# Performance work log

Measured on AMD Instinct MI355X. Metric: run time of the kernel, lower is better.

Reference implementation:

```python
import jax, jax.numpy as jnp
import numpy as np

B, S, D, H = 4, 2048, 1024, 16
HS = D // H  # head_size = 64
EPS = 1e-5


def setup_inputs() -> dict:
    key = jax.random.key(0)
    ks = jax.random.split(key, 10)
    s = 0.02
    return {
        "v": jax.random.normal(ks[0], (B, S, D), dtype=jnp.float32),
        "k": jax.random.normal(ks[1], (B, S, D), dtype=jnp.float32),
        "q": jax.random.normal(ks[2], (B, S, D), dtype=jnp.float32),
        "mask": jnp.triu(jnp.ones((S, S), dtype=bool), k=1),  # True = masked (causal)
        "ln_g": jnp.ones((D,), dtype=jnp.float32),
        "ln_b": jnp.zeros((D,), dtype=jnp.float32),
        # per-head projections, stacked: [H, D, HS]
        "Wq": jax.random.normal(ks[3], (H, D, HS), dtype=jnp.float32) * s,
        "Wk": jax.random.normal(ks[4], (H, D, HS), dtype=jnp.float32) * s,
        "Wv": jax.random.normal(ks[5], (H, D, HS), dtype=jnp.float32) * s,
        "Wp": jax.random.normal(ks[6], (D, D), dtype=jnp.float32) * s,
        "bp": jnp.zeros((D,), dtype=jnp.float32),
    }


def _layernorm(x, g, b):
    mu = jnp.mean(x, axis=-1, keepdims=True)
    var = jnp.var(x, axis=-1, keepdims=True)
    return (x - mu) * jax.lax.rsqrt(var + EPS) * g + b


def reference(v, k, q, mask, ln_g, ln_b, Wq, Wk, Wv, Wp, bp):
    v = _layernorm(v, ln_g, ln_b)
    k = _layernorm(k, ln_g, ln_b)
    q = _layernorm(q, ln_g, ln_b)
    # per-head projections: [B,S,D] x [H,D,E] -> [B,H,S,E]
    qh = jnp.einsum("bsd,hde->bhse", q, Wq)
    kh = jnp.einsum("bsd,hde->bhse", k, Wk)
    vh = jnp.einsum("bsd,hde->bhse", v, Wv)
    # NOTE: original scales by full embedding_dim C**-0.5 (not head_size)
    scale = jnp.float32(D) ** -0.5
    w = jnp.einsum("bhqe,bhke->bhqk", qh, kh) * scale
    w = jnp.where(mask, -jnp.inf, w)
    w = jax.nn.softmax(w, axis=-1)
    out = jnp.einsum("bhqk,bhke->bhqe", w, vh)  # [B,H,S,E]
    out = out.transpose(0, 2, 1, 3).reshape(B, S, D)  # concat heads
    return out @ Wp.T + bp
```

## Files before the change

### kernel.cpp

```cpp
#include <hip/hip_runtime.h>
#include <hip/hip_bf16.h>
#include <cstdint>
#include <cstddef>

#define Bq 4
#define Sq 2048
#define Dq 1024
#define Hq 16
#define HSq 64
#define Kc 1024

typedef short short8 __attribute__((ext_vector_type(8)));
typedef float f32x4 __attribute__((ext_vector_type(4)));

__device__ __forceinline__ unsigned short f2bf(float f){
  __hip_bfloat16 h = __float2bfloat16(f);
  return __builtin_bit_cast(unsigned short, h);
}

__device__ __forceinline__ float exp2hw(float x){
  float r;
  asm("v_exp_f32 %0, %1" : "=v"(r) : "v"(x));
  return r;
}
__device__ __forceinline__ unsigned cvtpk(float lo, float hi){
  unsigned r;
  asm("v_cvt_pk_bf16_f32 %0, %1, %2" : "=v"(r) : "v"(lo), "v"(hi));
  return r;
}
__device__ __forceinline__ float rcphw(float x){
  float r;
  asm("v_rcp_f32 %0, %1" : "=v"(r) : "v"(x));
  return r;
}

__device__ __forceinline__ void gl_lds16(const void* g, void* l){
  __builtin_amdgcn_global_load_lds((const __attribute__((address_space(1))) void*)(g),
                                   (__attribute__((address_space(3))) void*)(l), 16, 0, 0);
}

__global__ __launch_bounds__(256) void ln3_kernel(const float* __restrict__ v,
                                                  const float* __restrict__ k,
                                                  const float* __restrict__ q,
                                                  const float* __restrict__ g,
                                                  const float* __restrict__ bta,
                                                  short* __restrict__ vo,
                                                  short* __restrict__ ko,
                                                  short* __restrict__ qo){
  const int which = blockIdx.y;
  const float* x = (which==0) ? v : (which==1) ? k : q;
  short* out     = (which==0) ? vo : (which==1) ? ko : qo;
  const int row = blockIdx.x;
  const float* xr = x + (size_t)row * Dq;
  const int t = threadIdx.x;
  float4 vv = reinterpret_cast<const float4*>(xr)[t];
  float s  = vv.x + vv.y + vv.z + vv.w;
  float ss = vv.x*vv.x + vv.y*vv.y + vv.z*vv.z + vv.w*vv.w;
  #pragma unroll
  for (int o = 32; o >= 1; o >>= 1){ s += __shfl_xor(s, o); ss += __shfl_xor(ss, o); }
  __shared__ float red[8];
  const int wid = t >> 6;
  if ((t & 63) == 0){ red[wid] = s; red[4+wid] = ss; }
  __syncthreads();
  s  = red[0]+red[1]+red[2]+red[3];
  ss = red[4]+red[5]+red[6]+red[7];
  const float mu   = s * (1.0f/Dq);
  const float var  = ss * (1.0f/Dq) - mu*mu;
  const float rstd = rsqrtf(var + 1e-5f);
  float4 gv = reinterpret_cast<const float4*>(g)[t];
  float4 bv = reinterpret_cast<const float4*>(bta)[t];
  ushort4 o4;
  o4.x = f2bf((vv.x-mu)*rstd*gv.x + bv.x);
  o4.y = f2bf((vv.y-mu)*rstd*gv.y + bv.y);
  o4.z = f2bf((vv.z-mu)*rstd*gv.z + bv.z);
  o4.w = f2bf((vv.w-mu)*rstd*gv.w + bv.w);
  reinterpret_cast<ushort4*>(out + (size_t)row*Dq)[t] = o4;
}

__global__ __launch_bounds__(256) void cvt_kernel(const float* __restrict__ in,
                                                  short* __restrict__ out, int n4){
  int i = blockIdx.x*256 + threadIdx.x;
  if (i < n4){
    float4 v = reinterpret_cast<const float4*>(in)[i];
    ushort4 o; o.x=f2bf(v.x); o.y=f2bf(v.y); o.z=f2bf(v.z); o.w=f2bf(v.w);
    reinterpret_cast<ushort4*>(out)[i] = o;
  }
}

__global__ __launch_bounds__(256) void trcvt3_kernel(const float* __restrict__ Wq,
                                                     const float* __restrict__ Wk,
                                                     const float* __restrict__ Wv,
                                                     short* __restrict__ wqt,
                                                     short* __restrict__ wkt,
                                                     short* __restrict__ wvt){
  const int z = blockIdx.z;
  const float* Wsrc = (z==0) ? Wq : (z==1) ? Wk : Wv;
  short* Wdst       = (z==0) ? wqt : (z==1) ? wkt : wvt;
  const float scl   = (z==0) ? (0.03125f * 1.44269504f) : 1.0f;
  const int h = blockIdx.y, kt = blockIdx.x, tid = threadIdx.x;
  __shared__ short t[64][68];
  const float* src = Wsrc + ((size_t)h*Kc + (size_t)kt*64) * HSq;
  #pragma unroll
  for (int c=0;c<4;c++){
    int lin = c*256 + tid;
    int kr = lin >> 4;
    int e4 = (lin & 15) * 4;
    float4 vv = *reinterpret_cast<const float4*>(&src[(size_t)kr*HSq + e4]);
    t[e4+0][kr] = (short)f2bf(vv.x*scl);
    t[e4+1][kr] = (short)f2bf(vv.y*scl);
    t[e4+2][kr] = (short)f2bf(vv.z*scl);
    t[e4+3][kr] = (short)f2bf(vv.w*scl);
  }
  __syncthreads();
  short* dst = Wdst + (size_t)h*HSq*Kc + (size_t)kt*64;
  #pragma unroll
  for (int c=0;c<4;c++){
    int lin = c*256 + tid;
    int er = lin >> 4;
    int k4 = (lin & 15) * 4;
    ushort4 o;
    o.x = (unsigned short)t[er][k4+0];
    o.y = (unsigned short)t[er][k4+1];
    o.z = (unsigned short)t[er][k4+2];
    o.w = (unsigned short)t[er][k4+3];
    *reinterpret_cast<ushort4*>(&dst[(size_t)er*Kc + k4]) = o;
  }
}

__global__ __launch_bounds__(256) void proj3_kernel(
    const short* __restrict__ qn, const short* __restrict__ kn, const short* __restrict__ vn,
    const short* __restrict__ wqt, const short* __restrict__ wkt, const short* __restrict__ wvt,
    short* __restrict__ qh, short* __restrict__ kh, short* __restrict__ vhT)
{
  const int z = blockIdx.y;
  const short* A  = (z==0) ? qn  : (z==1) ? kn  : vn;
  const short* BT = (z==0) ? wqt : (z==1) ? wkt : wvt;

  const int bid = blockIdx.x;
  const int c8_ = bid & 7, j = bid >> 3;
  const int bm = c8_*8 + (j & 7), bn = j >> 3;
  const int m0 = bm * 128;
  const int n0c = bn * 128;
  const int tid = threadIdx.x;
  const int lane = tid & 63, w = tid >> 6;
  const int wm = w >> 1, wn = w & 1;
  const int fr = lane & 15, fg = lane >> 4;

  __shared__ short As[128*64];
  __shared__ short Bs[128*64];

  f32x4 acc[4][4] = {};

  const int rowT = tid >> 3;
  const int inb  = (tid & 7) * 16;

  for (int kt = 0; kt < Kc/64; ++kt){
    const int k0 = kt*64;
    #pragma unroll
    for (int c=0;c<4;c++){
      int row = c*32 + rowT;
      int src = inb ^ ((row & 7) << 4);
      gl_lds16((const char*)(A  + (size_t)(m0  + row)*Kc + k0) + src,
               (char*)As + c*4096 + w*1024);
      gl_lds16((const char*)(BT + (size_t)(n0c + row)*Kc + k0) + src,
               (char*)Bs + c*4096 + w*1024);
    }
    __syncthreads();
    #pragma unroll
    for (int kk=0;kk<2;kk++){
      short8 af[4], bf8[4];
      #pragma unroll
      for (int mr=0;mr<4;mr++){
        int row = wm*64 + mr*16 + fr;
        int byt = row*128 + ((kk*64 + fg*16) ^ ((row & 7) << 4));
        af[mr] = *reinterpret_cast<const short8*>((const char*)As + byt);
      }
      #pragma unroll
      for (int nr=0;nr<4;nr++){
        int row = wn*64 + nr*16 + fr;
        int byt = row*128 + ((kk*64 + fg*16) ^ ((row & 7) << 4));
        bf8[nr] = *reinterpret_cast<const short8*>((const char*)Bs + byt);
      }
      #pragma unroll
      for (int mr=0;mr<4;mr++)
        #pragma unroll
        for (int nr=0;nr<4;nr++)
          acc[mr][nr] = __builtin_amdgcn_mfma_f32_16x16x32_bf16(af[mr], bf8[nr], acc[mr][nr], 0, 0, 0);
    }
    __syncthreads();
  }

  if (z == 2){
    #pragma unroll
    for (int mr=0;mr<4;mr++){
      #pragma unroll
      for (int nr=0;nr<4;nr++){
        int col = n0c + wn*64 + nr*16 + fr;
        int h = col >> 6, e = col & 63;
        int R = m0 + wm*64 + mr*16 + fg*4;
        int bb = R >> 11, sPos = R & (Sq-1);
        uint2 o;
        o.x = cvtpk(acc[mr][nr][0], acc[mr][nr][1]);
        o.y = cvtpk(acc[mr][nr][2], acc[mr][nr][3]);
        *reinterpret_cast<uint2*>(&vhT[(((size_t)bb*Hq + h)*HSq + e)*Sq + sPos]) = o;
      }
    }
  } else {
    short* outb = z ? kh : qh;
    #pragma unroll
    for (int mr=0;mr<4;mr++){
      #pragma unroll
      for (int nr=0;nr<4;nr++){
        int col = n0c + wn*64 + nr*16 + fr;
        int h = col >> 6, e = col & 63;
        #pragma unroll
        for (int r=0;r<4;r++){
          int R = m0 + wm*64 + mr*16 + fg*4 + r;
          int bb = R >> 11, sPos = R & (Sq-1);
          outb[(((size_t)bb*Hq + h)*Sq + sPos)*HSq + e] = (short)f2bf(acc[mr][nr][r]);
        }
      }
    }
  }
}

__global__ __launch_bounds__(256) void gemmo_kernel(
    const short* __restrict__ A,
    const short* __restrict__ BT,
    const float* __restrict__ bias,
    float* __restrict__ outf)
{
  const int bid = blockIdx.x;
  const int c8_ = bid & 7, j = bid >> 3;
  const int bm = c8_*8 + (j & 7), bn = j >> 3;
  const int m0 = bm * 128;
  const int n0c = bn * 128;
  const int tid = threadIdx.x;
  const int lane = tid & 63, w = tid >> 6;
  const int wm = w >> 1, wn = w & 1;
  const int fr = lane & 15, fg = lane >> 4;

  __shared__ short As[128*64];
  __shared__ short Bs[128*64];

  f32x4 acc[4][4] = {};

  const int rowT = tid >> 3;
  const int inb  = (tid & 7) * 16;

  for (int kt = 0; kt < Kc/64; ++kt){
    const int k0 = kt*64;
    #pragma unroll
    for (int c=0;c<4;c++){
      int row = c*32 + rowT;
      int src = inb ^ ((row & 7) << 4);
      gl_lds16((const char*)(A  + (size_t)(m0  + row)*Kc + k0) + src,
               (char*)As + c*4096 + w*1024);
      gl_lds16((const char*)(BT + (size_t)(n0c + row)*Kc + k0) + src,
               (char*)Bs + c*4096 + w*1024);
    }
    __syncthreads();
    #pragma unroll
    for (int kk=0;kk<2;kk++){
      short8 af[4], bf8[4];
      #pragma unroll
      for (int mr=0;mr<4;mr++){
        int row = wm*64 + mr*16 + fr;
        int byt = row*128 + ((kk*64 + fg*16) ^ ((row & 7) << 4));
        af[mr] = *reinterpret_cast<const short8*>((const char*)As + byt);
      }
      #pragma unroll
      for (int nr=0;nr<4;nr++){
        int row = wn*64 + nr*16 + fr;
        int byt = row*128 + ((kk*64 + fg*16) ^ ((row & 7) << 4));
        bf8[nr] = *reinterpret_cast<const short8*>((const char*)Bs + byt);
      }
      #pragma unroll
      for (int mr=0;mr<4;mr++)
        #pragma unroll
        for (int nr=0;nr<4;nr++)
          acc[mr][nr] = __builtin_amdgcn_mfma_f32_16x16x32_bf16(af[mr], bf8[nr], acc[mr][nr], 0, 0, 0);
    }
    __syncthreads();
  }

  #pragma unroll
  for (int mr=0;mr<4;mr++){
    #pragma unroll
    for (int nr=0;nr<4;nr++){
      int col = n0c + wn*64 + nr*16 + fr;
      #pragma unroll
      for (int r=0;r<4;r++){
        int R = m0 + wm*64 + mr*16 + fg*4 + r;
        outf[(size_t)R*Dq + col] = acc[mr][nr][r] + bias[col];
      }
    }
  }
}

__global__ __launch_bounds__(256, 4) void attn_kernel(
    const short* __restrict__ qh, const short* __restrict__ kh,
    const short* __restrict__ vhT, short* __restrict__ attO)
{
  const int bid = blockIdx.x;
  const int jp  = bid >> 6;
  const int g   = bid & 63;
  const int h = g & 15, b = g >> 4;
  const short* Q  = qh  + (((size_t)b*Hq + h)*Sq)*HSq;
  const short* K  = kh  + (((size_t)b*Hq + h)*Sq)*HSq;
  const short* VT = vhT + (((size_t)b*Hq + h)*HSq)*Sq;
  const int tid = threadIdx.x, w = tid >> 6, lane = tid & 63;
  const int fr = lane & 15, fg = lane >> 4;

  __shared__ short KsB[2][64*64];
  __shared__ short VtB[2][64*64];
  __shared__ short Ps[4][32][76];

  const int sRow = tid >> 3;
  const int swz  = ((tid & 7) << 4) ^ ((sRow & 7) << 4);
  const char* pK = (const char*)K  + (size_t)sRow*128      + swz;
  const char* pV = (const char*)VT + (size_t)sRow*(Sq*2)   + swz;

  short8 ones;
  #pragma unroll
  for (int i=0;i<8;i++) ones[i] = (short)0x3F80;

  for (int pass = 0; pass < 2; ++pass){
    const int qt = pass ? jp : (15 - jp);
    const int qbase = qt * 128;
    const int nkv = 2*qt + 2;

    short8 qa[2][2];
    #pragma unroll
    for (int mr=0;mr<2;mr++){
      const int qrow = qbase + w*32 + mr*16 + fr;
      #pragma unroll
      for (int kk=0;kk<2;kk++)
        qa[mr][kk] = *reinterpret_cast<const short8*>(&Q[(size_t)qrow*HSq + kk*32 + 8*fg]);
    }

    f32x4 accO[2][4] = {};
    f32x4 accL[2] = {};

    #pragma unroll
    for (int c=0;c<2;c++){
      gl_lds16(pK + c*4096,   (char*)KsB[0] + c*4096 + w*1024);
      gl_lds16(pV + c*131072, (char*)VtB[0] + c*4096 + w*1024);
    }
    __syncthreads();

    for (int kt0 = 0; kt0 < nkv; kt0 += 2){
      #pragma unroll
      for (int u = 0; u < 2; ++u){
        const int kt = kt0 + u;
        const int buf = u;

        if (kt+1 < nkv){
          const char* nK = pK + (size_t)(kt+1)*8192;
          const char* nV = pV + (size_t)(kt+1)*128;
          #pragma unroll
          for (int c=0;c<2;c++){
            gl_lds16(nK + c*4096,   (char*)KsB[buf^1] + c*4096 + w*1024);
            gl_lds16(nV + c*131072, (char*)VtB[buf^1] + c*4096 + w*1024);
          }
        }

        f32x4 sfr[2][4] = {};
        __builtin_amdgcn_s_setprio(1);
        #pragma unroll
        for (int kk=0;kk<2;kk++){
          short8 kb[4];
          #pragma unroll
          for (int n0=0;n0<4;n0++){
            int row = n0*16 + fr;
            int byt = row*128 + ((((kk*4+fg) ^ (row & 7))) << 4);
            kb[n0] = *reinterpret_cast<const short8*>((const char*)KsB[buf] + byt);
          }
          #pragma unroll
          for (int mr=0;mr<2;mr++)
            #pragma unroll
            for (int n0=0;n0<4;n0++)
              sfr[mr][n0] = __builtin_amdgcn_mfma_f32_16x16x32_bf16(kb[n0], qa[mr][kk], sfr[mr][n0], 0, 0, 0);
        }
        __builtin_amdgcn_s_setprio(0);

        #pragma unroll
        for (int mr=0;mr<2;mr++){
          const int qr = qbase + w*32 + mr*16 + fr;
          const bool needmask = (kt*64 + 63) > (qbase + w*32 + mr*16);
          #pragma unroll
          for (int n0=0;n0<4;n0++){
            float p0 = exp2hw(sfr[mr][n0][0]);
            float p1 = exp2hw(sfr[mr][n0][1]);
            float p2 = exp2hw(sfr[mr][n0][2]);
            float p3 = exp2hw(sfr[mr][n0][3]);
            if (needmask){
              int kc = kt*64 + n0*16 + fg*4;
              if (kc+0 > qr) p0 = 0.0f;
              if (kc+1 > qr) p1 = 0.0f;
              if (kc+2 > qr) p2 = 0.0f;
              if (kc+3 > qr) p3 = 0.0f;
            }
            uint2 u2;
            u2.x = cvtpk(p0, p1);
            u2.y = cvtpk(p2, p3);
            *reinterpret_cast<uint2*>(&Ps[w][mr*16 + fr][n0*16 + fg*4]) = u2;
          }
        }

        __builtin_amdgcn_s_setprio(1);
        #pragma unroll
        for (int kk=0;kk<2;kk++){
          short8 pa[2], vb[4];
          #pragma unroll
          for (int mr=0;mr<2;mr++)
            pa[mr] = *reinterpret_cast<short8*>(&Ps[w][mr*16 + fr][kk*32 + 8*fg]);
          #pragma unroll
          for (int n0=0;n0<4;n0++){
            int row = n0*16 + fr;
            int byt = row*128 + ((((kk*4+fg) ^ (row & 7))) << 4);
            vb[n0] = *reinterpret_cast<const short8*>((const char*)VtB[buf] + byt);
          }
          #pragma unroll
          for (int mr=0;mr<2;mr++){
            #pragma unroll
            for (int n0=0;n0<4;n0++)
              accO[mr][n0] = __builtin_amdgcn_mfma_f32_16x16x32_bf16(vb[n0], pa[mr], accO[mr][n0], 0, 0, 0);
            accL[mr] = __builtin_amdgcn_mfma_f32_16x16x32_bf16(ones, pa[mr], accL[mr], 0, 0, 0);
          }
        }
        __builtin_amdgcn_s_setprio(0);

        __syncthreads();
      }
    }

    #pragma unroll
    for (int mr=0;mr<2;mr++){
      float inv = rcphw(accL[mr][0]);
      const int qr = qbase + w*32 + mr*16 + fr;
      short* orow = attO + ((size_t)b*Sq + qr)*Dq + h*HSq;
      #pragma unroll
      for (int n0=0;n0<4;n0++){
        uint2 u2;
        u2.x = cvtpk(accO[mr][n0][0] * inv, accO[mr][n0][1] * inv);
        u2.y = cvtpk(accO[mr][n0][2] * inv, accO[mr][n0][3] * inv);
        *reinterpret_cast<uint2*>(&orow[n0*16 + fg*4]) = u2;
      }
    }
  }
}

extern "C" void kernel_launch(void* const* d_in, const int* in_sizes, int n_in,
                              void* d_out, int out_size, void* d_ws, size_t ws_size,
                              hipStream_t stream){
  const float* v_in = (const float*)d_in[0];
  const float* k_in = (const float*)d_in[1];
  const float* q_in = (const float*)d_in[2];
  const float* ln_g = (const float*)d_in[4];
  const float* ln_b = (const float*)d_in[5];
  const float* Wq   = (const float*)d_in[6];
  const float* Wk   = (const float*)d_in[7];
  const float* Wv   = (const float*)d_in[8];
  const float* Wp   = (const float*)d_in[9];
  const float* bp   = (const float*)d_in[10];
  float* out = (float*)d_out;

  char* ws = (char*)d_ws;
  const size_t BSD  = (size_t)Bq*Sq*Dq;
  const size_t BSD2 = BSD * 2;
  short* vn  = (short*)(ws);
  short* kn  = (short*)(ws + BSD2);
  short* qn  = (short*)(ws + 2*BSD2);
  short* wqt = (short*)(ws + 3*BSD2);
  short* wkt = (short*)(ws + 3*BSD2 + 2097152);
  short* wvt = (short*)(ws + 3*BSD2 + 2*2097152);
  short* wpb = (short*)(ws + 3*BSD2 + 3*2097152);
  short* qh  = (short*)(ws + 3*BSD2 + 4*2097152);
  short* kh  = qh + BSD;
  short* vhT = kh + BSD;
  short* attO = vn;

  ln3_kernel<<<dim3(Bq*Sq, 3), 256, 0, stream>>>(v_in, k_in, q_in, ln_g, ln_b, vn, kn, qn);

  trcvt3_kernel<<<dim3(16, Hq, 3), 256, 0, stream>>>(Wq, Wk, Wv, wqt, wkt, wvt);
  cvt_kernel<<<1024, 256, 0, stream>>>(Wp, wpb, 262144);

  proj3_kernel<<<dim3(512, 3), 256, 0, stream>>>(qn, kn, vn, wqt, wkt, wvt, qh, kh, vhT);

  attn_kernel<<<512, 256, 0, stream>>>(qh, kh, vhT, attO);

  gemmo_kernel<<<512, 256, 0, stream>>>(attO, wpb, bp, out);
}
```

Baseline: 186.3 us.

## Rewrite projection GEMM with 256x256 tiles, 512 threads and double-buffered LDS pipeline

```diff
diff --git a/kernel.cpp b/kernel.cpp
--- a/kernel.cpp
+++ b/kernel.cpp
@@ -127,7 +127,7 @@
   }
 }
 
-__global__ __launch_bounds__(256) void proj3_kernel(
+__global__ __launch_bounds__(512, 2) void proj3_kernel(
     const short* __restrict__ qn, const short* __restrict__ kn, const short* __restrict__ vn,
     const short* __restrict__ wqt, const short* __restrict__ wkt, const short* __restrict__ wvt,
     short* __restrict__ qh, short* __restrict__ kh, short* __restrict__ vhT)
@@ -136,88 +136,120 @@
   const short* A  = (z==0) ? qn  : (z==1) ? kn  : vn;
   const short* BT = (z==0) ? wqt : (z==1) ? wkt : wvt;
 
-  const int bid = blockIdx.x;
-  const int c8_ = bid & 7, j = bid >> 3;
-  const int bm = c8_*8 + (j & 7), bn = j >> 3;
-  const int m0 = bm * 128;
-  const int n0c = bn * 128;
+  const int i = blockIdx.x;
+  const int bm = i & 31, bn = i >> 5;
+  const int m0 = bm * 256;
+  const int n0c = bn * 256;
   const int tid = threadIdx.x;
   const int lane = tid & 63, w = tid >> 6;
-  const int wm = w >> 1, wn = w & 1;
+  const int wm = w >> 2, wn = w & 3;
   const int fr = lane & 15, fg = lane >> 4;
 
-  __shared__ short As[128*64];
-  __shared__ short Bs[128*64];
-
-  f32x4 acc[4][4] = {};
-
-  const int rowT = tid >> 3;
-  const int inb  = (tid & 7) * 16;
-
-  for (int kt = 0; kt < Kc/64; ++kt){
-    const int k0 = kt*64;
-    #pragma unroll
-    for (int c=0;c<4;c++){
-      int row = c*32 + rowT;
-      int src = inb ^ ((row & 7) << 4);
-      gl_lds16((const char*)(A  + (size_t)(m0  + row)*Kc + k0) + src,
-               (char*)As + c*4096 + w*1024);
-      gl_lds16((const char*)(BT + (size_t)(n0c + row)*Kc + k0) + src,
-               (char*)Bs + c*4096 + w*1024);
-    }
-    __syncthreads();
-    #pragma unroll
-    for (int kk=0;kk<2;kk++){
-      short8 af[4], bf8[4];
-      #pragma unroll
-      for (int mr=0;mr<4;mr++){
-        int row = wm*64 + mr*16 + fr;
-        int byt = row*128 + ((kk*64 + fg*16) ^ ((row & 7) << 4));
-        af[mr] = *reinterpret_cast<const short8*>((const char*)As + byt);
-      }
-      #pragma unroll
-      for (int nr=0;nr<4;nr++){
-        int row = wn*64 + nr*16 + fr;
-        int byt = row*128 + ((kk*64 + fg*16) ^ ((row & 7) << 4));
-        bf8[nr] = *reinterpret_cast<const short8*>((const char*)Bs + byt);
-      }
-      #pragma unroll
-      for (int mr=0;mr<4;mr++)
-        #pragma unroll
-        for (int nr=0;nr<4;nr++)
-          acc[mr][nr] = __builtin_amdgcn_mfma_f32_16x16x32_bf16(af[mr], bf8[nr], acc[mr][nr], 0, 0, 0);
-    }
-    __syncthreads();
-  }
+  __shared__ short As[2*256*64];
+  __shared__ short Bs[2*256*64];
+
+  f32x4 acc[8][4] = {};
+  short8 bf[4][2];
+
+  const int srow = tid >> 3;
+  const int sw   = ((tid & 7) << 4) ^ ((srow & 7) << 4);
+  const char* aB = (const char*)(A  + (size_t)(m0  + srow)*Kc) + sw;
+  const char* bB = (const char*)(BT + (size_t)(n0c + srow)*Kc) + sw;
+
+#define STAGE(t, hh, buf) do{                                              \
+    const bool isB_ = (hh) < 2;                                            \
+    const char* s_ = (isB_ ? bB : aB) + (size_t)((hh)&1)*(128*2048) + (size_t)(t)*128; \
+    char* d_ = (char*)(isB_ ? (void*)Bs : (void*)As) + (buf)*32768 + ((hh)&1)*16384 + w*1024; \
+    gl_lds16(s_, d_);                                                      \
+    gl_lds16(s_ + 64*2048, d_ + 8192);                                     \
+  }while(0)
+
+#define READ_A(p, buf, af) do{                                             \
+    _Pragma("unroll") for (int mm=0; mm<2; ++mm){                          \
+      const int r_ = ((p)*2+mm)*32 + wm*16 + fr;                           \
+      _Pragma("unroll") for (int kk=0; kk<2; ++kk){                        \
+        const int byt_ = (buf)*32768 + r_*128 + (((kk*4+fg)^(r_&7))<<4);   \
+        af[mm][kk] = *reinterpret_cast<const short8*>((const char*)As + byt_); \
+      }}}while(0)
+
+#define MFMA_P(p, af) do{                                                  \
+    __builtin_amdgcn_s_setprio(1);                                         \
+    _Pragma("unroll") for (int kk=0; kk<2; ++kk)                           \
+      _Pragma("unroll") for (int mm=0; mm<2; ++mm)                         \
+        _Pragma("unroll") for (int nr=0; nr<4; ++nr)                       \
+          acc[(p)*2+mm][nr] = __builtin_amdgcn_mfma_f32_16x16x32_bf16(af[mm][kk], bf[nr][kk], acc[(p)*2+mm][nr], 0, 0, 0); \
+    __builtin_amdgcn_s_setprio(0);                                         \
+  }while(0)
+
+#define DO_TILE(t, buf, HN) do{                                            \
+    asm volatile("s_waitcnt vmcnt(2)" ::: "memory");                       \
+    __builtin_amdgcn_s_barrier();                                          \
+    _Pragma("unroll") for (int nr=0; nr<4; ++nr){                          \
+      const int r_ = wn*64 + nr*16 + fr;                                   \
+      _Pragma("unroll") for (int kk=0; kk<2; ++kk){                        \
+        const int byt_ = (buf)*32768 + r_*128 + (((kk*4+fg)^(r_&7))<<4);   \
+        bf[nr][kk] = *reinterpret_cast<const short8*>((const char*)Bs + byt_); \
+      }}                                                                   \
+    { short8 af[2][2]; READ_A(0, buf, af);                                 \
+      if (HN) STAGE((t)+1, 0, (buf)^1);                                    \
+      MFMA_P(0, af); }                                                     \
+    { short8 af[2][2]; READ_A(1, buf, af);                                 \
+      if (HN) STAGE((t)+1, 1, (buf)^1);                                    \
+      MFMA_P(1, af); }                                                     \
+    if (HN) { asm volatile("s_waitcnt vmcnt(4)" ::: "memory"); }           \
+    else    { asm volatile("s_waitcnt vmcnt(0)" ::: "memory"); }           \
+    __builtin_amdgcn_s_barrier();                                          \
+    { short8 af[2][2]; READ_A(2, buf, af);                                 \
+      if (HN) STAGE((t)+1, 2, (buf)^1);                                    \
+      MFMA_P(2, af); }                                                     \
+    { short8 af[2][2]; READ_A(3, buf, af);                                 \
+      if (HN) STAGE((t)+1, 3, (buf)^1);                                    \
+      MFMA_P(3, af); }                                                     \
+  }while(0)
+
+  STAGE(0, 0, 0); STAGE(0, 1, 0); STAGE(0, 2, 0); STAGE(0, 3, 0);
+
+  for (int t2 = 0; t2 < 7; ++t2){
+    const int t = t2*2;
+    DO_TILE(t,   0, true);
+    DO_TILE(t+1, 1, true);
+  }
+  DO_TILE(14, 0, true);
+  DO_TILE(15, 1, false);
+
+#undef DO_TILE
+#undef MFMA_P
+#undef READ_A
+#undef STAGE
 
   if (z == 2){
     #pragma unroll
-    for (int mr=0;mr<4;mr++){
-      #pragma unroll
-      for (int nr=0;nr<4;nr++){
+    for (int mi=0; mi<8; ++mi){
+      #pragma unroll
+      for (int nr=0; nr<4; ++nr){
         int col = n0c + wn*64 + nr*16 + fr;
         int h = col >> 6, e = col & 63;
-        int R = m0 + wm*64 + mr*16 + fg*4;
+        int R = m0 + mi*32 + wm*16 + fg*4;
         int bb = R >> 11, sPos = R & (Sq-1);
         uint2 o;
-        o.x = cvtpk(acc[mr][nr][0], acc[mr][nr][1]);
-        o.y = cvtpk(acc[mr][nr][2], acc[mr][nr][3]);
+        o.x = cvtpk(acc[mi][nr][0], acc[mi][nr][1]);
+        o.y = cvtpk(acc[mi][nr][2], acc[mi][nr][3]);
         *reinterpret_cast<uint2*>(&vhT[(((size_t)bb*Hq + h)*HSq + e)*Sq + sPos]) = o;
       }
     }
   } else {
     short* outb = z ? kh : qh;
     #pragma unroll
-    for (int mr=0;mr<4;mr++){
-      #pragma unroll
-      for (int nr=0;nr<4;nr++){
+    for (int mi=0; mi<8; ++mi){
+      #pragma unroll
+      for (int nr=0; nr<4; ++nr){
         int col = n0c + wn*64 + nr*16 + fr;
         int h = col >> 6, e = col & 63;
         #pragma unroll
-        for (int r=0;r<4;r++){
-          int R = m0 + wm*64 + mr*16 + fg*4 + r;
+        for (int r=0; r<4; ++r){
+          int R = m0 + mi*32 + wm*16 + fg*4 + r;
           int bb = R >> 11, sPos = R & (Sq-1);
-          outb[(((size_t)bb*Hq + h)*Sq + sPos)*HSq + e] = (short)f2bf(acc[mr][nr][r]);
+          outb[(((size_t)bb*Hq + h)*Sq + sPos)*HSq + e] = (short)f2bf(acc[mi][nr][r]);
         }
       }
     }
@@ -323,7 +355,7 @@
 
   short8 ones;
   #pragma unroll
-  for (int i=0;i<8;i++) ones[i] = (short)0x3F80;
+  for (int ii=0;ii<8;ii++) ones[ii] = (short)0x3F80;
 
   for (int pass = 0; pass < 2; ++pass){
     const int qt = pass ? jp : (15 - jp);
@@ -486,7 +518,7 @@
   trcvt3_kernel<<<dim3(16, Hq, 3), 256, 0, stream>>>(Wq, Wk, Wv, wqt, wkt, wvt);
   cvt_kernel<<<1024, 256, 0, stream>>>(Wp, wpb, 262144);
 
-  proj3_kernel<<<dim3(512, 3), 256, 0, stream>>>(qn, kn, vn, wqt, wkt, wvt, qh, kh, vhT);
+  proj3_kernel<<<dim3(128, 3), 512, 0, stream>>>(qn, kn, vn, wqt, wkt, wvt, qh, kh, vhT);
 
   attn_kernel<<<512, 256, 0, stream>>>(qh, kh, vhT, attO);
 
```

Measured after the change: 182.6 us (median of 2 runs). -2.0%, faster.

## Enlarge QKV projection GEMM tiles to 256x256 with 512-thread blocks

Applied to the files above, without the earlier changes.

```diff
diff --git a/kernel.cpp b/kernel.cpp
--- a/kernel.cpp
+++ b/kernel.cpp
@@ -127,7 +127,7 @@
   }
 }
 
-__global__ __launch_bounds__(256) void proj3_kernel(
+__global__ __launch_bounds__(512, 4) void proj3_kernel(
     const short* __restrict__ qn, const short* __restrict__ kn, const short* __restrict__ vn,
     const short* __restrict__ wqt, const short* __restrict__ wkt, const short* __restrict__ wvt,
     short* __restrict__ qh, short* __restrict__ kh, short* __restrict__ vhT)
@@ -136,68 +136,65 @@
   const short* A  = (z==0) ? qn  : (z==1) ? kn  : vn;
   const short* BT = (z==0) ? wqt : (z==1) ? wkt : wvt;
 
-  const int bid = blockIdx.x;
-  const int c8_ = bid & 7, j = bid >> 3;
-  const int bm = c8_*8 + (j & 7), bn = j >> 3;
-  const int m0 = bm * 128;
-  const int n0c = bn * 128;
+  const int i = blockIdx.x;
+  const int bm = i & 31, bn = i >> 5;
+  const int m0 = bm * 256;
+  const int n0c = bn * 256;
   const int tid = threadIdx.x;
   const int lane = tid & 63, w = tid >> 6;
-  const int wm = w >> 1, wn = w & 1;
+  const int wm = w >> 2, wn = w & 3;
   const int fr = lane & 15, fg = lane >> 4;
 
-  __shared__ short As[128*64];
-  __shared__ short Bs[128*64];
-
-  f32x4 acc[4][4] = {};
-
-  const int rowT = tid >> 3;
-  const int inb  = (tid & 7) * 16;
-
-  for (int kt = 0; kt < Kc/64; ++kt){
-    const int k0 = kt*64;
+  __shared__ short As[256*64];
+  __shared__ short Bs[256*64];
+
+  f32x4 acc[8][4] = {};
+
+  const int srow = tid >> 3;
+  const int sw   = ((tid & 7) << 4) ^ ((srow & 7) << 4);
+  const char* aB = (const char*)(A  + (size_t)(m0  + srow)*Kc) + sw;
+  const char* bB = (const char*)(BT + (size_t)(n0c + srow)*Kc) + sw;
+
+  for (int kt = 0; kt < 16; ++kt){
+    const size_t koff = (size_t)kt * 128;
     #pragma unroll
     for (int c=0;c<4;c++){
-      int row = c*32 + rowT;
-      int src = inb ^ ((row & 7) << 4);
-      gl_lds16((const char*)(A  + (size_t)(m0  + row)*Kc + k0) + src,
-               (char*)As + c*4096 + w*1024);
-      gl_lds16((const char*)(BT + (size_t)(n0c + row)*Kc + k0) + src,
-               (char*)Bs + c*4096 + w*1024);
+      gl_lds16(aB + (size_t)c*131072 + koff, (char*)As + c*8192 + w*1024);
+      gl_lds16(bB + (size_t)c*131072 + koff, (char*)Bs + c*8192 + w*1024);
     }
     __syncthreads();
     #pragma unroll
     for (int kk=0;kk<2;kk++){
-      short8 af[4], bf8[4];
-      #pragma unroll
-      for (int mr=0;mr<4;mr++){
-        int row = wm*64 + mr*16 + fr;
-        int byt = row*128 + ((kk*64 + fg*16) ^ ((row & 7) << 4));
-        af[mr] = *reinterpret_cast<const short8*>((const char*)As + byt);
-      }
+      short8 bf8[4];
       #pragma unroll
       for (int nr=0;nr<4;nr++){
         int row = wn*64 + nr*16 + fr;
-        int byt = row*128 + ((kk*64 + fg*16) ^ ((row & 7) << 4));
+        int byt = row*128 + (((kk*4+fg) ^ (row & 7)) << 4);
         bf8[nr] = *reinterpret_cast<const short8*>((const char*)Bs + byt);
       }
-      #pragma unroll
-      for (int mr=0;mr<4;mr++)
+      __builtin_amdgcn_s_setprio(1);
+      #pragma unroll
+      for (int mr=0;mr<8;mr++){
+        int row = wm*128 + mr*16 + fr;
+        int byt = row*128 + (((kk*4+fg) ^ (row & 7)) << 4);
+        short8 a = *reinterpret_cast<const short8*>((const char*)As + byt);
         #pragma unroll
         for (int nr=0;nr<4;nr++)
-          acc[mr][nr] = __builtin_amdgcn_mfma_f32_16x16x32_bf16(af[mr], bf8[nr], acc[mr][nr], 0, 0, 0);
+          acc[mr][nr] = __builtin_amdgcn_mfma_f32_16x16x32_bf16(a, bf8[nr], acc[mr][nr], 0, 0, 0);
+      }
+      __builtin_amdgcn_s_setprio(0);
     }
     __syncthreads();
   }
 
   if (z == 2){
     #pragma unroll
-    for (int mr=0;mr<4;mr++){
-      #pragma unroll
-      for (int nr=0;nr<4;nr++){
+    for (int mr=0; mr<8; ++mr){
+      #pragma unroll
+      for (int nr=0; nr<4; ++nr){
         int col = n0c + wn*64 + nr*16 + fr;
         int h = col >> 6, e = col & 63;
-        int R = m0 + wm*64 + mr*16 + fg*4;
+        int R = m0 + wm*128 + mr*16 + fg*4;
         int bb = R >> 11, sPos = R & (Sq-1);
         uint2 o;
         o.x = cvtpk(acc[mr][nr][0], acc[mr][nr][1]);
@@ -208,14 +205,14 @@
   } else {
     short* outb = z ? kh : qh;
     #pragma unroll
-    for (int mr=0;mr<4;mr++){
-      #pragma unroll
-      for (int nr=0;nr<4;nr++){
+    for (int mr=0; mr<8; ++mr){
+      #pragma unroll
+      for (int nr=0; nr<4; ++nr){
         int col = n0c + wn*64 + nr*16 + fr;
         int h = col >> 6, e = col & 63;
         #pragma unroll
-        for (int r=0;r<4;r++){
-          int R = m0 + wm*64 + mr*16 + fg*4 + r;
+        for (int r=0; r<4; ++r){
+          int R = m0 + wm*128 + mr*16 + fg*4 + r;
           int bb = R >> 11, sPos = R & (Sq-1);
           outb[(((size_t)bb*Hq + h)*Sq + sPos)*HSq + e] = (short)f2bf(acc[mr][nr][r]);
         }
@@ -323,7 +320,7 @@
 
   short8 ones;
   #pragma unroll
-  for (int i=0;i<8;i++) ones[i] = (short)0x3F80;
+  for (int ii=0;ii<8;ii++) ones[ii] = (short)0x3F80;
 
   for (int pass = 0; pass < 2; ++pass){
     const int qt = pass ? jp : (15 - jp);
@@ -486,7 +483,7 @@
   trcvt3_kernel<<<dim3(16, Hq, 3), 256, 0, stream>>>(Wq, Wk, Wv, wqt, wkt, wvt);
   cvt_kernel<<<1024, 256, 0, stream>>>(Wp, wpb, 262144);
 
-  proj3_kernel<<<dim3(512, 3), 256, 0, stream>>>(qn, kn, vn, wqt, wkt, wvt, qh, kh, vhT);
+  proj3_kernel<<<dim3(128, 3), 512, 0, stream>>>(qn, kn, vn, wqt, wkt, wvt, qh, kh, vhT);
 
   attn_kernel<<<512, 256, 0, stream>>>(qh, kh, vhT, attO);
 
```

New measurement: 397.6 us. 2.13x slower.
